# Kernel optimization log

Hardware: AMD Instinct MI355X
Metric: run time of the kernel (lower is better)

The kernel has to match this reference:

```python
import jax, jax.numpy as jnp
import numpy as np

RHO = 1.0          # ADMM penalty
LAM = 0.1          # lambda_sparse
MAX_ITERS = 20
ZETA = 0.05        # APAS drift threshold / CDS temperature
TAU = 0.1          # chiral stabilizer tolerance
STEP = 0.1         # gradient step size
COHESION = 1.0     # Mohr-Coulomb cohesion
MU = 0.5           # Mohr-Coulomb friction coefficient
DP_K = 10.0        # Drucker-Prager deviatoric-norm radius


def _pas(c):
    # Phase Alignment Invariant: scalar phase-coherence metric in [0,1]
    return jnp.abs(jnp.mean(jnp.cos(c)))


def _chirality(c):
    # odd (sign-sensitive) global moment
    return jnp.mean(c ** 3)


def _mc_proj(c, g):
    # Mohr-Coulomb yield projection: clamp magnitude to cohesion + mu*|grad|
    return jnp.sign(c) * jnp.minimum(jnp.abs(c), COHESION + MU * jnp.abs(g))


def _dp_proj(c):
    # Drucker-Prager: project deviatoric part onto norm ball of radius DP_K (per row)
    m = jnp.mean(c, axis=-1, keepdims=True)
    dev = c - m
    n = jnp.linalg.norm(dev, axis=-1, keepdims=True)
    scale = jnp.minimum(1.0, DP_K / (n + 1e-8))
    return m + dev * scale


def setup_inputs() -> dict:
    key = jax.random.key(0)
    k1, k2, k3 = jax.random.split(key, 3)
    B, D = 1024, 2048
    initial_c = 0.5 * jax.random.normal(k1, (B, D), dtype=jnp.float32)
    W = jax.random.normal(k2, (D, D), dtype=jnp.float32) / np.float32(np.sqrt(D))
    love_w = 1.0 + 0.01 * jax.random.normal(k3, (D,), dtype=jnp.float32)
    love_b = jnp.zeros((D,), dtype=jnp.float32)
    return {"initial_c": initial_c, "W": W, "love_w": love_w, "love_b": love_b}


def _forward(initial_c, W, love_w, love_b):
    c_sym = initial_c
    c0 = initial_c
    z0 = c0
    u0 = jnp.zeros_like(c0)
    prev_pas0 = _pas(c0)
    prev_score0 = -_chirality(c0)  # drift = 0 -> exp(0) = 1

    def step(carry, _):
        c, z, u, prev_pas, prev_score, low, done = carry

        def energy(ci):
            pred = ci @ W  # forward_op_fn
            violation_pressure = 0.5 * jnp.sum((pred - ci) ** 2)
            admm_tension = 0.5 * RHO * jnp.sum((ci - z + u) ** 2)
            return violation_pressure + admm_tension

        g = jax.grad(energy)(c)
        c_yield = _mc_proj(c, g)
        c_next = (c_yield * love_w + love_b) - STEP * g  # LoveVector then step
        z_in = c_next + u
        thr = LAM / RHO
        z_next = jnp.sign(z_in) * jnp.maximum(jnp.abs(z_in) - thr, 0.0)
        u_next = u + (c_next - z_next)

        cur_pas = _pas(c_next)
        drift = jnp.abs(cur_pas - prev_pas)
        violation = drift > ZETA
        low = jnp.where(cur_pas < 0.5, low + 1, 0)
        done = done | (low > 20)
        cur_score = -_chirality(c_next) * jnp.exp(-drift / ZETA)
        stable = (cur_score - prev_score) >= -TAU
        acc = (~violation) & stable & (~done)

        sel = lambda a, b: jnp.where(acc, a, b)
        new = (sel(c_next, c), sel(z_next, z), sel(u_next, u),
               jnp.where(acc, cur_pas, prev_pas),
               jnp.where(acc, cur_score, prev_score), low, done)
        return new, None

    init = (c0, z0, u0, prev_pas0, prev_score0,
            jnp.zeros((), jnp.int32), jnp.zeros((), jnp.bool_))
    (c_phys, z, u, _, _, _, _), _ = jax.lax.scan(step, init, None, length=MAX_ITERS)

    diff = jnp.linalg.norm(c_phys - c_sym)
    chi_cur = _chirality(c_phys)
    chi_orig = _chirality(c_sym)
    status = jnp.where(jnp.sign(chi_cur) != jnp.sign(chi_orig),
                       2,
                       jnp.where(diff > 5.0, 2, jnp.where(diff > 1.0, 1, 0))).astype(jnp.int32)

    delta = c_phys - c_sym
    symbolic_delta = jnp.round(delta * 10.0) / 10.0
    c_compressed = _dp_proj(c_sym + symbolic_delta)
    return c_compressed, status


def reference(initial_c, W, love_w, love_b):
    return _forward(initial_c, W, love_w, love_b)
```

## Files before the change

kernel.cpp:

```cpp
#include <hip/hip_runtime.h>
#include <math.h>

#define D 2048
#define BROWS 1024
#define NEL (D*BROWS)
#define NBLK 1024
#define NTHREADS_TOT (NBLK*256)

#define BM 128
#define BN 128
#define BK 16

__device__ __forceinline__ double blk_reduce(double v, double* sm) {
    const int t = threadIdx.x;
    sm[t] = v;
    __syncthreads();
    for (int s = 128; s > 0; s >>= 1) {
        if (t < s) sm[t] += sm[t + s];
        __syncthreads();
    }
    double r = sm[0];
    __syncthreads();
    return r;
}

__global__ __launch_bounds__(256) void k_gemm_nt(const float* __restrict__ A,
        const float* __restrict__ Bm, float* __restrict__ out0, float* __restrict__ out1,
        const float* __restrict__ Wadj, int ksz, int mode, const int* __restrict__ frz)
{
    if (frz && *frz) return;
    __shared__ float As[BK][BM + 4];
    __shared__ float Bs[BK][BN + 4];
    const int t  = threadIdx.x;
    const int tx = t & 15, ty = t >> 4;
    const int row0 = blockIdx.y * BM, col0 = blockIdx.x * BN;
    const int k0 = blockIdx.z * ksz;
    float* out = blockIdx.z ? out1 : out0;

    float acc[8][8];
    #pragma unroll
    for (int i = 0; i < 8; ++i)
        #pragma unroll
        for (int j = 0; j < 8; ++j) acc[i][j] = 0.0f;

    for (int kt = 0; kt < ksz; kt += BK) {
        #pragma unroll
        for (int v = 0; v < 2; ++v) {
            const int vid = t + v * 256;
            const int r = vid >> 2, cq = vid & 3;
            const float4 ga = *reinterpret_cast<const float4*>(
                &A[(size_t)(row0 + r) * D + (k0 + kt + cq * 4)]);
            As[cq*4+0][r] = ga.x; As[cq*4+1][r] = ga.y;
            As[cq*4+2][r] = ga.z; As[cq*4+3][r] = ga.w;
            const float4 gb = *reinterpret_cast<const float4*>(
                &Bm[(size_t)(col0 + r) * D + (k0 + kt + cq * 4)]);
            Bs[cq*4+0][r] = gb.x; Bs[cq*4+1][r] = gb.y;
            Bs[cq*4+2][r] = gb.z; Bs[cq*4+3][r] = gb.w;
        }
        __syncthreads();
        #pragma unroll
        for (int k = 0; k < BK; ++k) {
            float a[8], b[8];
            *reinterpret_cast<float4*>(&a[0]) = *reinterpret_cast<const float4*>(&As[k][ty*4]);
            *reinterpret_cast<float4*>(&a[4]) = *reinterpret_cast<const float4*>(&As[k][ty*4+64]);
            *reinterpret_cast<float4*>(&b[0]) = *reinterpret_cast<const float4*>(&Bs[k][tx*4]);
            *reinterpret_cast<float4*>(&b[4]) = *reinterpret_cast<const float4*>(&Bs[k][tx*4+64]);
            #pragma unroll
            for (int i = 0; i < 8; ++i)
                #pragma unroll
                for (int j = 0; j < 8; ++j)
                    acc[i][j] += a[i] * b[j];
        }
        __syncthreads();
    }

    #pragma unroll
    for (int i = 0; i < 8; ++i) {
        const int grow = row0 + ((i < 4) ? (ty*4 + i) : (64 + ty*4 + i - 4));
        float vv[8];
        #pragma unroll
        for (int j = 0; j < 8; ++j) vv[j] = acc[i][j];
        if (mode == 0) {
            #pragma unroll
            for (int j = 0; j < 8; ++j) {
                const int gcol = col0 + ((j < 4) ? (tx*4 + j) : (64 + tx*4 + j - 4));
                const float wsum = Wadj[(size_t)grow * D + gcol] + Wadj[(size_t)gcol * D + grow];
                vv[j] += (grow == gcol ? 1.0f : 0.0f) - wsum;
            }
        }
        const float4 o0 = make_float4(vv[0], vv[1], vv[2], vv[3]);
        const float4 o1 = make_float4(vv[4], vv[5], vv[6], vv[7]);
        *reinterpret_cast<float4*>(&out[(size_t)grow * D + col0 + tx*4])      = o0;
        *reinterpret_cast<float4*>(&out[(size_t)grow * D + col0 + 64 + tx*4]) = o1;
    }
}

__global__ __launch_bounds__(256) void k_init(const float* __restrict__ c0,
        float* __restrict__ c, float* __restrict__ z, float* __restrict__ u,
        double* __restrict__ partials)
{
    __shared__ double sm[256];
    double sc = 0.0, s3 = 0.0;
    const int tid = blockIdx.x * 256 + threadIdx.x;
    for (int i = tid; i < NEL; i += NTHREADS_TOT) {
        const float v = c0[i];
        c[i] = v; z[i] = v; u[i] = 0.0f;
        sc += (double)cosf(v);
        s3 += (double)((v * v) * v);
    }
    const double tc = blk_reduce(sc, sm);
    const double t3 = blk_reduce(s3, sm);
    if (threadIdx.x == 0) { partials[blockIdx.x] = tc; partials[NBLK + blockIdx.x] = t3; }
}

__global__ __launch_bounds__(256) void k_decide0(const double* __restrict__ partials,
        double* __restrict__ scal, int* __restrict__ flag, int* __restrict__ frz)
{
    __shared__ double sm[256];
    const int t = threadIdx.x;
    const double a = partials[t] + partials[t+256] + partials[t+512] + partials[t+768];
    const double b = partials[NBLK+t] + partials[NBLK+t+256] + partials[NBLK+t+512] + partials[NBLK+t+768];
    const double tc = blk_reduce(a, sm);
    const double t3 = blk_reduce(b, sm);
    if (t == 0) {
        const double pas = fabs(tc / (double)NEL);
        const double chi = t3 / (double)NEL;
        scal[0] = pas;
        scal[1] = -chi;
        scal[2] = chi;
        *flag = 0;
        *frz = 0;
    }
}

__global__ __launch_bounds__(256) void k_elem(float* __restrict__ P0g,
        const float* __restrict__ P1, const float* __restrict__ c,
        const float* __restrict__ z, const float* __restrict__ u,
        const float* __restrict__ lw, const float* __restrict__ lb,
        double* __restrict__ partials, const int* __restrict__ frz)
{
#pragma clang fp contract(off)
    if (*frz) return;
    __shared__ double sm[256];
    double sc = 0.0, s3 = 0.0;
    const int tid = blockIdx.x * 256 + threadIdx.x;
    for (int i = tid; i < NEL; i += NTHREADS_TOT) {
        const int j = i & (D - 1);
        const float cv = c[i];
        const float g = (P0g[i] + P1[i]) + ((cv - z[i]) + u[i]);
        const float lim = 1.0f + 0.5f * fabsf(g);
        const float mn = fminf(fabsf(cv), lim);
        const float cy = (cv > 0.0f) ? mn : ((cv < 0.0f) ? -mn : 0.0f);
        const float cnv = (cy * lw[j] + lb[j]) - 0.1f * g;
        P0g[i] = cnv;
        sc += (double)cosf(cnv);
        s3 += (double)((cnv * cnv) * cnv);
    }
    const double tc = blk_reduce(sc, sm);
    const double t3 = blk_reduce(s3, sm);
    if (threadIdx.x == 0) { partials[blockIdx.x] = tc; partials[NBLK + blockIdx.x] = t3; }
}

__global__ __launch_bounds__(256) void k_decide(const double* __restrict__ partials,
        double* __restrict__ scal, int* __restrict__ flag, int* __restrict__ frz)
{
    __shared__ double sm[256];
    if (*frz) return;
    const int t = threadIdx.x;
    const double a = partials[t] + partials[t+256] + partials[t+512] + partials[t+768];
    const double b = partials[NBLK+t] + partials[NBLK+t+256] + partials[NBLK+t+512] + partials[NBLK+t+768];
    const double tc = blk_reduce(a, sm);
    const double t3 = blk_reduce(b, sm);
    if (t == 0) {
        const double pas = fabs(tc / (double)NEL);
        const double drift = fabs(pas - scal[0]);
        const double chi = t3 / (double)NEL;
        const double score = -chi * exp(-drift / 0.05);
        const bool violation = drift > 0.05;
        const bool stable = (score - scal[1]) >= -0.1;
        const int acc = (!violation && stable) ? 1 : 0;
        *flag = acc;
        if (acc) { scal[0] = pas; scal[1] = score; }
        else     { *frz = 1; }
    }
}

__global__ __launch_bounds__(256) void k_commit(const float* __restrict__ cn,
        float* __restrict__ c, float* __restrict__ z, float* __restrict__ u,
        const int* __restrict__ flag)
{
#pragma clang fp contract(off)
    if (*flag == 0) return;
    const int tid = blockIdx.x * 256 + threadIdx.x;
    for (int i = tid; i < NEL; i += NTHREADS_TOT) {
        const float cnv = cn[i];
        const float uv = u[i];
        const float zi = cnv + uv;
        float zm = fabsf(zi) - 0.1f;
        zm = fmaxf(zm, 0.0f);
        const float zn = (zi > 0.0f) ? zm : ((zi < 0.0f) ? -zm : 0.0f);
        c[i] = cnv;
        z[i] = zn;
        u[i] = uv + (cnv - zn);
    }
}

__global__ __launch_bounds__(256) void k_final_rows(const float* __restrict__ c0,
        const float* __restrict__ c, float* __restrict__ outp)
{
#pragma clang fp contract(off)
    __shared__ double sm[256];
    const int row = blockIdx.x;
    const size_t base = (size_t)row * D;
    float tv[8];
    double s1 = 0.0;
    #pragma unroll
    for (int s = 0; s < 8; ++s) {
        const int j = threadIdx.x + s * 256;
        const float s0 = c0[base + j];
        const float delta = c[base + j] - s0;
        const float sym = rintf(delta * 10.0f) / 10.0f;
        const float tval = s0 + sym;
        tv[s] = tval;
        s1 += (double)tval;
    }
    const double tot = blk_reduce(s1, sm);
    const float m = (float)(tot / (double)D);
    double s2 = 0.0;
    #pragma unroll
    for (int s = 0; s < 8; ++s) {
        const float dev = tv[s] - m;
        s2 += (double)(dev * dev);
    }
    const double tot2 = blk_reduce(s2, sm);
    const float n = sqrtf((float)tot2);
    const float scale = fminf(1.0f, 10.0f / (n + 1e-8f));
    #pragma unroll
    for (int s = 0; s < 8; ++s) {
        const int j = threadIdx.x + s * 256;
        outp[base + j] = m + (tv[s] - m) * scale;
    }
}

__global__ __launch_bounds__(256) void k_final_glob(const float* __restrict__ c0,
        const float* __restrict__ c, double* __restrict__ partials)
{
    __shared__ double sm[256];
    double s3 = 0.0, sd = 0.0;
    const int tid = blockIdx.x * 256 + threadIdx.x;
    for (int i = tid; i < NEL; i += NTHREADS_TOT) {
        const float v = c[i];
        s3 += (double)((v * v) * v);
        const float d = v - c0[i];
        sd += (double)(d * d);
    }
    const double t3 = blk_reduce(s3, sm);
    const double td = blk_reduce(sd, sm);
    if (threadIdx.x == 0) { partials[blockIdx.x] = t3; partials[NBLK + blockIdx.x] = td; }
}

__global__ __launch_bounds__(256) void k_final_status(const double* __restrict__ partials,
        const double* __restrict__ scal, float* __restrict__ outp)
{
    __shared__ double sm[256];
    const int t = threadIdx.x;
    const double a = partials[t] + partials[t+256] + partials[t+512] + partials[t+768];
    const double b = partials[NBLK+t] + partials[NBLK+t+256] + partials[NBLK+t+512] + partials[NBLK+t+768];
    const double t3 = blk_reduce(a, sm);
    const double td = blk_reduce(b, sm);
    if (t == 0) {
        const double chi_cur = t3 / (double)NEL;
        const double diff = sqrt(td);
        const double chi_orig = scal[2];
        const int s_cur = (chi_cur > 0.0) - (chi_cur < 0.0);
        const int s_org = (chi_orig > 0.0) - (chi_orig < 0.0);
        int status;
        if (s_cur != s_org)   status = 2;
        else if (diff > 5.0)  status = 2;
        else if (diff > 1.0)  status = 1;
        else                  status = 0;
        outp[NEL] = (float)status;
    }
}

extern "C" void kernel_launch(void* const* d_in, const int* in_sizes, int n_in,
                              void* d_out, int out_size, void* d_ws, size_t ws_size,
                              hipStream_t stream)
{
    const float* c0 = (const float*)d_in[0];
    const float* W  = (const float*)d_in[1];
    const float* lw = (const float*)d_in[2];
    const float* lb = (const float*)d_in[3];
    float* outp = (float*)d_out;

    float* Mbuf = (float*)d_ws;
    float* c  = Mbuf + (size_t)D * D;
    float* z  = c + NEL;
    float* u  = z + NEL;
    float* P0 = u + NEL;
    float* P1 = P0 + NEL;
    double* partials = (double*)(P1 + NEL);
    double* scal = partials + 2 * NBLK;
    int* flag = (int*)(scal + 4);
    int* frz  = flag + 1;

    k_gemm_nt<<<dim3(D / BN, D / BM, 1), 256, 0, stream>>>(W, W, Mbuf, Mbuf, W, D, 0, nullptr);
    k_init<<<NBLK, 256, 0, stream>>>(c0, c, z, u, partials);
    k_decide0<<<1, 256, 0, stream>>>(partials, scal, flag, frz);

    for (int it = 0; it < 20; ++it) {
        k_gemm_nt<<<dim3(D / BN, BROWS / BM, 2), 256, 0, stream>>>(c, Mbuf, P0, P1, nullptr, D / 2, 1, frz);
        k_elem<<<NBLK, 256, 0, stream>>>(P0, P1, c, z, u, lw, lb, partials, frz);
        k_decide<<<1, 256, 0, stream>>>(partials, scal, flag, frz);
        k_commit<<<NBLK, 256, 0, stream>>>(P0, c, z, u, flag);
    }

    k_final_rows<<<BROWS, 256, 0, stream>>>(c0, c, outp);
    k_final_glob<<<NBLK, 256, 0, stream>>>(c0, c, partials);
    k_final_status<<<1, 256, 0, stream>>>(partials, scal, outp);
}
```

Measured before the change: 3.028 ms.

## Ping-pong state buffers to drop commit pass and shrink GEMM row tile

The per-iteration commit kernel is removed by double-buffering c. The fused elementwise kernel now writes c_next into the alternate buffer and updates z and u in place, while the decide kernel records which buffer holds the accepted state. Overwriting z and u before the accept decision is safe only because a rejection freezes all later iterations and the final kernels read only c. Separately, the GEMM tile changes from 128x128 to 64x128, doubling the block count to improve CU occupancy at the cost of less operand reuse per block. The ping-pong path runs only when the workspace has room for one extra state buffer; otherwise the old path is kept.

```diff
diff --git a/kernel.cpp b/kernel.cpp
--- a/kernel.cpp
+++ b/kernel.cpp
@@ -7,9 +7,9 @@
 #define NBLK 1024
 #define NTHREADS_TOT (NBLK*256)
 
-#define BM 128
-#define BN 128
-#define BK 16
+#define GM 64
+#define GN 128
+#define GK 16
 
 __device__ __forceinline__ double blk_reduce(double v, double* sm) {
     const int t = threadIdx.x;
@@ -24,59 +24,59 @@
     return r;
 }
 
-__global__ __launch_bounds__(256) void k_gemm_nt(const float* __restrict__ A,
-        const float* __restrict__ Bm, float* __restrict__ out0, float* __restrict__ out1,
+__global__ __launch_bounds__(256) void k_gemm(const float* __restrict__ A,
+        const float* __restrict__ B, float* __restrict__ P0, float* __restrict__ P1,
         const float* __restrict__ Wadj, int ksz, int mode, const int* __restrict__ frz)
 {
     if (frz && *frz) return;
-    __shared__ float As[BK][BM + 4];
-    __shared__ float Bs[BK][BN + 4];
+    __shared__ float As[GK][GM + 4];
+    __shared__ float Bs[GK][GN + 4];
     const int t  = threadIdx.x;
     const int tx = t & 15, ty = t >> 4;
-    const int row0 = blockIdx.y * BM, col0 = blockIdx.x * BN;
+    const int row0 = blockIdx.y * GM, col0 = blockIdx.x * GN;
     const int k0 = blockIdx.z * ksz;
-    float* out = blockIdx.z ? out1 : out0;
-
-    float acc[8][8];
-    #pragma unroll
-    for (int i = 0; i < 8; ++i)
+    float* __restrict__ out = blockIdx.z ? P1 : P0;
+
+    float acc[4][8];
+    #pragma unroll
+    for (int i = 0; i < 4; ++i)
         #pragma unroll
         for (int j = 0; j < 8; ++j) acc[i][j] = 0.0f;
 
-    for (int kt = 0; kt < ksz; kt += BK) {
+    const int ra = t >> 2, ca = t & 3;
+    for (int kt = 0; kt < ksz; kt += GK) {
+        const int kb = k0 + kt;
+        const float4 ga = *reinterpret_cast<const float4*>(
+            &A[(size_t)(row0 + ra) * D + kb + ca * 4]);
+        As[ca*4+0][ra] = ga.x; As[ca*4+1][ra] = ga.y;
+        As[ca*4+2][ra] = ga.z; As[ca*4+3][ra] = ga.w;
         #pragma unroll
         for (int v = 0; v < 2; ++v) {
             const int vid = t + v * 256;
-            const int r = vid >> 2, cq = vid & 3;
-            const float4 ga = *reinterpret_cast<const float4*>(
-                &A[(size_t)(row0 + r) * D + (k0 + kt + cq * 4)]);
-            As[cq*4+0][r] = ga.x; As[cq*4+1][r] = ga.y;
-            As[cq*4+2][r] = ga.z; As[cq*4+3][r] = ga.w;
+            const int rb = vid >> 2, cb = vid & 3;
             const float4 gb = *reinterpret_cast<const float4*>(
-                &Bm[(size_t)(col0 + r) * D + (k0 + kt + cq * 4)]);
-            Bs[cq*4+0][r] = gb.x; Bs[cq*4+1][r] = gb.y;
-            Bs[cq*4+2][r] = gb.z; Bs[cq*4+3][r] = gb.w;
+                &B[(size_t)(col0 + rb) * D + kb + cb * 4]);
+            Bs[cb*4+0][rb] = gb.x; Bs[cb*4+1][rb] = gb.y;
+            Bs[cb*4+2][rb] = gb.z; Bs[cb*4+3][rb] = gb.w;
         }
         __syncthreads();
         #pragma unroll
-        for (int k = 0; k < BK; ++k) {
-            float a[8], b[8];
+        for (int k = 0; k < GK; ++k) {
+            float a[4], b[8];
             *reinterpret_cast<float4*>(&a[0]) = *reinterpret_cast<const float4*>(&As[k][ty*4]);
-            *reinterpret_cast<float4*>(&a[4]) = *reinterpret_cast<const float4*>(&As[k][ty*4+64]);
             *reinterpret_cast<float4*>(&b[0]) = *reinterpret_cast<const float4*>(&Bs[k][tx*4]);
-            *reinterpret_cast<float4*>(&b[4]) = *reinterpret_cast<const float4*>(&Bs[k][tx*4+64]);
+            *reinterpret_cast<float4*>(&b[4]) = *reinterpret_cast<const float4*>(&Bs[k][64 + tx*4]);
             #pragma unroll
-            for (int i = 0; i < 8; ++i)
+            for (int i = 0; i < 4; ++i)
                 #pragma unroll
                 for (int j = 0; j < 8; ++j)
                     acc[i][j] += a[i] * b[j];
         }
         __syncthreads();
     }
-
-    #pragma unroll
-    for (int i = 0; i < 8; ++i) {
-        const int grow = row0 + ((i < 4) ? (ty*4 + i) : (64 + ty*4 + i - 4));
+    #pragma unroll
+    for (int i = 0; i < 4; ++i) {
+        const int grow = row0 + ty*4 + i;
         float vv[8];
         #pragma unroll
         for (int j = 0; j < 8; ++j) vv[j] = acc[i][j];
@@ -88,10 +88,11 @@
                 vv[j] += (grow == gcol ? 1.0f : 0.0f) - wsum;
             }
         }
-        const float4 o0 = make_float4(vv[0], vv[1], vv[2], vv[3]);
-        const float4 o1 = make_float4(vv[4], vv[5], vv[6], vv[7]);
-        *reinterpret_cast<float4*>(&out[(size_t)grow * D + col0 + tx*4])      = o0;
-        *reinterpret_cast<float4*>(&out[(size_t)grow * D + col0 + 64 + tx*4]) = o1;
+        float* orow = &out[(size_t)grow * D + col0];
+        *reinterpret_cast<float4*>(&orow[tx*4]) =
+            make_float4(vv[0], vv[1], vv[2], vv[3]);
+        *reinterpret_cast<float4*>(&orow[64 + tx*4]) =
+            make_float4(vv[4], vv[5], vv[6], vv[7]);
     }
 }
 
@@ -114,7 +115,8 @@
 }
 
 __global__ __launch_bounds__(256) void k_decide0(const double* __restrict__ partials,
-        double* __restrict__ scal, int* __restrict__ flag, int* __restrict__ frz)
+        double* __restrict__ scal, int* __restrict__ flag, int* __restrict__ frz,
+        int* __restrict__ sel)
 {
     __shared__ double sm[256];
     const int t = threadIdx.x;
@@ -125,15 +127,48 @@
     if (t == 0) {
         const double pas = fabs(tc / (double)NEL);
         const double chi = t3 / (double)NEL;
-        scal[0] = pas;
-        scal[1] = -chi;
-        scal[2] = chi;
-        *flag = 0;
-        *frz = 0;
-    }
-}
-
-__global__ __launch_bounds__(256) void k_elem(float* __restrict__ P0g,
+        scal[0] = pas; scal[1] = -chi; scal[2] = chi;
+        *flag = 0; *frz = 0; *sel = 0;
+    }
+}
+
+__global__ __launch_bounds__(256) void k_elem_pp(const float* __restrict__ P0,
+        const float* __restrict__ P1, const float* __restrict__ cc,
+        float* __restrict__ cn, float* __restrict__ z, float* __restrict__ u,
+        const float* __restrict__ lw, const float* __restrict__ lb,
+        double* __restrict__ partials, const int* __restrict__ frz)
+{
+#pragma clang fp contract(off)
+    if (*frz) return;
+    __shared__ double sm[256];
+    double sc = 0.0, s3 = 0.0;
+    const int tid = blockIdx.x * 256 + threadIdx.x;
+    for (int i = tid; i < NEL; i += NTHREADS_TOT) {
+        const int j = i & (D - 1);
+        const float cv = cc[i];
+        const float zv = z[i];
+        const float uv = u[i];
+        const float g = (P0[i] + P1[i]) + ((cv - zv) + uv);
+        const float lim = 1.0f + 0.5f * fabsf(g);
+        const float mn = fminf(fabsf(cv), lim);
+        const float cy = (cv > 0.0f) ? mn : ((cv < 0.0f) ? -mn : 0.0f);
+        const float cnv = (cy * lw[j] + lb[j]) - 0.1f * g;
+        cn[i] = cnv;
+        const float zi = cnv + uv;
+        float zm = fabsf(zi) - 0.1f;
+        zm = fmaxf(zm, 0.0f);
+        const float zn = (zi > 0.0f) ? zm : ((zi < 0.0f) ? -zm : 0.0f);
+        z[i] = zn;
+        u[i] = uv + (cnv - zn);
+        sc += (double)cosf(cnv);
+        s3 += (double)((cnv * cnv) * cnv);
+    }
+    const double tc = blk_reduce(sc, sm);
+    const double t3 = blk_reduce(s3, sm);
+    if (threadIdx.x == 0) { partials[blockIdx.x] = tc; partials[NBLK + blockIdx.x] = t3; }
+}
+
+__global__ __launch_bounds__(256) void k_elem(float* __restrict__ P0,
         const float* __restrict__ P1, const float* __restrict__ c,
         const float* __restrict__ z, const float* __restrict__ u,
         const float* __restrict__ lw, const float* __restrict__ lb,
@@ -147,12 +182,12 @@
     for (int i = tid; i < NEL; i += NTHREADS_TOT) {
         const int j = i & (D - 1);
         const float cv = c[i];
-        const float g = (P0g[i] + P1[i]) + ((cv - z[i]) + u[i]);
+        const float g = (P0[i] + P1[i]) + ((cv - z[i]) + u[i]);
         const float lim = 1.0f + 0.5f * fabsf(g);
         const float mn = fminf(fabsf(cv), lim);
         const float cy = (cv > 0.0f) ? mn : ((cv < 0.0f) ? -mn : 0.0f);
         const float cnv = (cy * lw[j] + lb[j]) - 0.1f * g;
-        P0g[i] = cnv;
+        P0[i] = cnv;
         sc += (double)cosf(cnv);
         s3 += (double)((cnv * cnv) * cnv);
     }
@@ -162,7 +197,8 @@
 }
 
 __global__ __launch_bounds__(256) void k_decide(const double* __restrict__ partials,
-        double* __restrict__ scal, int* __restrict__ flag, int* __restrict__ frz)
+        double* __restrict__ scal, int* __restrict__ flag, int* __restrict__ frz,
+        int* __restrict__ sel, int next_sel)
 {
     __shared__ double sm[256];
     if (*frz) return;
@@ -180,7 +216,7 @@
         const bool stable = (score - scal[1]) >= -0.1;
         const int acc = (!violation && stable) ? 1 : 0;
         *flag = acc;
-        if (acc) { scal[0] = pas; scal[1] = score; }
+        if (acc) { scal[0] = pas; scal[1] = score; *sel = next_sel; }
         else     { *frz = 1; }
     }
 }
@@ -206,10 +242,12 @@
 }
 
 __global__ __launch_bounds__(256) void k_final_rows(const float* __restrict__ c0,
-        const float* __restrict__ c, float* __restrict__ outp)
+        const float* __restrict__ cA, const float* __restrict__ cB,
+        const int* __restrict__ sel, float* __restrict__ outp)
 {
 #pragma clang fp contract(off)
     __shared__ double sm[256];
+    const float* __restrict__ c = (*sel) ? cB : cA;
     const int row = blockIdx.x;
     const size_t base = (size_t)row * D;
     float tv[8];
@@ -243,9 +281,11 @@
 }
 
 __global__ __launch_bounds__(256) void k_final_glob(const float* __restrict__ c0,
-        const float* __restrict__ c, double* __restrict__ partials)
-{
-    __shared__ double sm[256];
+        const float* __restrict__ cA, const float* __restrict__ cB,
+        const int* __restrict__ sel, double* __restrict__ partials)
+{
+    __shared__ double sm[256];
+    const float* __restrict__ c = (*sel) ? cB : cA;
     double s3 = 0.0, sd = 0.0;
     const int tid = blockIdx.x * 256 + threadIdx.x;
     for (int i = tid; i < NEL; i += NTHREADS_TOT) {
@@ -293,29 +333,42 @@
     const float* lb = (const float*)d_in[3];
     float* outp = (float*)d_out;
 
-    float* Mbuf = (float*)d_ws;
-    float* c  = Mbuf + (size_t)D * D;
-    float* z  = c + NEL;
-    float* u  = z + NEL;
-    float* P0 = u + NEL;
-    float* P1 = P0 + NEL;
-    double* partials = (double*)(P1 + NEL);
+    const size_t M4 = (size_t)D * D;
+    const size_t N4 = (size_t)NEL;
+    float* Mb = (float*)d_ws;
+    float* region = Mb + M4;
+
+    const size_t tail_bytes = (2 * NBLK + 8) * sizeof(double) + 4 * sizeof(int);
+    const bool pp = ws_size >= (M4 + 6 * N4) * sizeof(float) + tail_bytes;
+
+    float *cA, *cB, *z, *u, *P0, *P1;
+    if (pp) { cA = region; cB = cA + N4; z = cB + N4; u = z + N4; P0 = u + N4; P1 = P0 + N4; }
+    else    { cA = region; cB = cA;      z = cA + N4; u = z + N4; P0 = u + N4; P1 = P0 + N4; }
+    double* partials = (double*)(P1 + N4);
     double* scal = partials + 2 * NBLK;
-    int* flag = (int*)(scal + 4);
+    int* flag = (int*)(scal + 8);
     int* frz  = flag + 1;
-
-    k_gemm_nt<<<dim3(D / BN, D / BM, 1), 256, 0, stream>>>(W, W, Mbuf, Mbuf, W, D, 0, nullptr);
-    k_init<<<NBLK, 256, 0, stream>>>(c0, c, z, u, partials);
-    k_decide0<<<1, 256, 0, stream>>>(partials, scal, flag, frz);
-
-    for (int it = 0; it < 20; ++it) {
-        k_gemm_nt<<<dim3(D / BN, BROWS / BM, 2), 256, 0, stream>>>(c, Mbuf, P0, P1, nullptr, D / 2, 1, frz);
-        k_elem<<<NBLK, 256, 0, stream>>>(P0, P1, c, z, u, lw, lb, partials, frz);
-        k_decide<<<1, 256, 0, stream>>>(partials, scal, flag, frz);
-        k_commit<<<NBLK, 256, 0, stream>>>(P0, c, z, u, flag);
-    }
-
-    k_final_rows<<<BROWS, 256, 0, stream>>>(c0, c, outp);
-    k_final_glob<<<NBLK, 256, 0, stream>>>(c0, c, partials);
+    int* sel  = frz + 1;
+
+    k_gemm<<<dim3(D / GN, D / GM, 1), 256, 0, stream>>>(W, W, Mb, Mb, W, D, 0, nullptr);
+    k_init<<<NBLK, 256, 0, stream>>>(c0, cA, z, u, partials);
+    k_decide0<<<1, 256, 0, stream>>>(partials, scal, flag, frz, sel);
+
+    for (int t = 0; t < 20; ++t) {
+        const float* ccur = (pp && (t & 1)) ? cB : cA;
+        float* cnxt = (pp && !(t & 1)) ? cB : cA;
+        k_gemm<<<dim3(D / GN, BROWS / GM, 2), 256, 0, stream>>>(ccur, Mb, P0, P1, nullptr, D / 2, 1, frz);
+        if (pp) {
+            k_elem_pp<<<NBLK, 256, 0, stream>>>(P0, P1, ccur, cnxt, z, u, lw, lb, partials, frz);
+            k_decide<<<1, 256, 0, stream>>>(partials, scal, flag, frz, sel, (t + 1) & 1);
+        } else {
+            k_elem<<<NBLK, 256, 0, stream>>>(P0, P1, cA, z, u, lw, lb, partials, frz);
+            k_decide<<<1, 256, 0, stream>>>(partials, scal, flag, frz, sel, 0);
+            k_commit<<<NBLK, 256, 0, stream>>>(P0, cA, z, u, flag);
+        }
+    }
+
+    k_final_rows<<<BROWS, 256, 0, stream>>>(c0, cA, cB, sel, outp);
+    k_final_glob<<<NBLK, 256, 0, stream>>>(c0, cA, cB, sel, partials);
     k_final_status<<<1, 256, 0, stream>>>(partials, scal, outp);
 }
```

Measured after the change: 2.911 ms. -3.9%, faster.
